# Performance work log

Hardware: AMD Instinct MI355X
Metric: run time of the kernel (lower is better)

The kernel has to match this reference:

```python
import jax, jax.numpy as jnp
import numpy as np

B, D = 8, 256
N_LIVE, K_NEW = 10000, 32
KC = N_LIVE + K_NEW
N_SAMPLES = 100
EPSILON = 0.1


def setup_inputs() -> dict:
    key = jax.random.key(0)
    k1, k2, k3, k4, k5, k6 = jax.random.split(key, 6)
    return {
        "xt": jax.random.normal(k1, (B, D), dtype=jnp.float32),
        "live_x0": jax.random.normal(k2, (B, N_LIVE, D), dtype=jnp.float32),
        "live_ll": jax.random.normal(k3, (B, N_LIVE, 1), dtype=jnp.float32),
        "x0": jax.random.normal(k4, (B, K_NEW, D), dtype=jnp.float32),
        "ll": jax.random.normal(k5, (B, K_NEW, 1), dtype=jnp.float32),
        "t_scale": jnp.float32(0.5),
        "boot_idx": jax.random.randint(k6, (N_SAMPLES, B, KC), 0, KC, dtype=jnp.int32),
    }


def reference(xt, live_x0, live_ll, x0, ll, t_scale, boot_idx):
    # --- spotlight_score core math ---
    # gaussian correction for the new particles: 0.5*||x0-xt||^2/sigma^2 + log(sigma)
    diff_new = x0 - xt[:, None, :]                                   # [B,K,D]
    corr_new = 0.5 * jnp.sum(diff_new ** 2, axis=-1, keepdims=True) / t_scale ** 2  # [B,K,1]
    current_x0 = jnp.concatenate([live_x0, x0], axis=1)              # [B,Kc,D]
    current_ll = jnp.concatenate(
        [live_ll, ll + corr_new + jnp.log(t_scale)], axis=1)         # [B,Kc,1]

    diff = current_x0 - xt[:, None, :]                               # [B,Kc,D]
    use_ll = (current_ll
              - 0.5 * jnp.sum(diff ** 2, axis=-1, keepdims=True) / t_scale ** 2
              - jnp.log(t_scale))                                    # [B,Kc,1]

    scores_p = diff / t_scale                                        # [B,Kc,D] per-particle scores
    logits = use_ll[..., 0]                                          # [B,Kc]

    # --- check_convergence: bootstrap resampled softmax reductions ---
    def body(carry, idx_n):                                          # idx_n: [B,Kc]
        s = jnp.take_along_axis(scores_p, idx_n[:, :, None], axis=1)  # [B,Kc,D]
        l = jnp.take_along_axis(logits, idx_n, axis=1)                # [B,Kc]
        w = jax.nn.softmax(l, axis=1)
        return carry, jnp.einsum('bk,bkd->bd', w, s)                  # [B,D]

    _, boot = jax.lax.scan(body, None, boot_idx)                      # [N,B,D]
    sigma_v = jnp.std(boot, axis=0, ddof=1)                           # [B,D] (torch.std is unbiased)
    converged = jnp.all(sigma_v < EPSILON * t_scale, axis=1)          # [B]

    # --- final importance-weighted score ---
    w = jax.nn.softmax(logits, axis=1)                                # [B,Kc]
    score = jnp.einsum('bk,bkd->bd', w, scores_p)                     # [B,D]
    return score, converged
```

## Files before the change

kernel.cpp:

```cpp
#include <hip/hip_runtime.h>
#include <math.h>

#define B 8
#define D 256
#define N_LIVE 10000
#define K_NEW 32
#define KC 10032
#define NS 100
#define NROW 101
#define EPS 0.1f
#define CAP 1024
#define ACT_CUT 87.0f
#define LBLK 314
#define BMAX_STRIDE 320

#define WS_HDR    0
#define WS_BMAX   160
#define WS_LOGITS (WS_BMAX + B * BMAX_STRIDE)
#define WS_ACTE   (WS_LOGITS + B * KC)
#define WS_ACTI   (WS_ACTE + B * CAP)
#define WS_LUT    (WS_ACTI + B * CAP)
#define WS_BOOT   (WS_LUT + B * KC / 2)


__global__ __launch_bounds__(256) void k_logits(
    const float* __restrict__ xt, const float* __restrict__ live_x0,
    const float* __restrict__ live_ll, const float* __restrict__ x0n,
    const float* __restrict__ lln, const float* __restrict__ ts_p,
    float* __restrict__ logits, float* __restrict__ bmax,
    unsigned* __restrict__ hdr) {
  int b = blockIdx.y;
  if (blockIdx.x == 0 && threadIdx.x == 0) hdr[128 + b] = 0;
  int w = threadIdx.x >> 6;
  int lane = threadIdx.x & 63;
  int k0 = blockIdx.x * 32 + w * 8;
  bool valid = (k0 < KC);
  int kb = valid ? k0 : 0;
  float4 c = ((const float4*)(xt + b * D))[lane];

  float s[8];
#pragma unroll
  for (int p = 0; p < 8; p++) {
    int k = kb + p;
    const float* src = (k < N_LIVE)
        ? (live_x0 + ((size_t)b * N_LIVE + k) * D)
        : (x0n + ((size_t)b * K_NEW + (k - N_LIVE)) * D);
    float4 v = ((const float4*)src)[lane];
    float dx = v.x - c.x, dy = v.y - c.y, dz = v.z - c.z, dw = v.w - c.w;
    s[p] = dx * dx + dy * dy + dz * dz + dw * dw;
  }
#pragma unroll
  for (int off = 32; off; off >>= 1) {
#pragma unroll
    for (int p = 0; p < 8; p++) s[p] += __shfl_xor(s[p], off);
  }
  __shared__ float wlog[4];
  if (lane == 0) {
    float ts = *ts_p;
    float inv2 = 0.5f / (ts * ts), lts = logf(ts);
    float o[8];
#pragma unroll
    for (int p = 0; p < 8; p++) {
      int k = kb + p;
      o[p] = (k < N_LIVE)
          ? live_ll[(size_t)b * N_LIVE + k] - s[p] * inv2 - lts
          : lln[(size_t)b * K_NEW + (k - N_LIVE)];
    }
    if (valid) {
      float4 o0 = {o[0], o[1], o[2], o[3]}, o1 = {o[4], o[5], o[6], o[7]};
      *(float4*)(logits + (size_t)b * KC + kb) = o0;
      *(float4*)(logits + (size_t)b * KC + kb + 4) = o1;
      wlog[w] = fmaxf(fmaxf(fmaxf(o[0], o[1]), fmaxf(o[2], o[3])),
                      fmaxf(fmaxf(o[4], o[5]), fmaxf(o[6], o[7])));
    } else {
      wlog[w] = -INFINITY;
    }
  }
  __syncthreads();
  if (threadIdx.x == 0)
    bmax[b * BMAX_STRIDE + blockIdx.x] =
        fmaxf(fmaxf(wlog[0], wlog[1]), fmaxf(wlog[2], wlog[3]));
}

__global__ __launch_bounds__(256) void k_select(
    const float* __restrict__ logits, const float* __restrict__ bmax,
    unsigned* __restrict__ hdr, float* __restrict__ act_e,
    int* __restrict__ act_idx, unsigned short* __restrict__ lut) {
  int b = blockIdx.y;
  __shared__ float sm[4];
  float m = -INFINITY;
  for (int i = threadIdx.x; i < LBLK; i += 256)
    m = fmaxf(m, bmax[b * BMAX_STRIDE + i]);
#pragma unroll
  for (int off = 32; off; off >>= 1) m = fmaxf(m, __shfl_xor(m, off));
  if ((threadIdx.x & 63) == 0) sm[threadIdx.x >> 6] = m;
  __syncthreads();
  float M = fmaxf(fmaxf(sm[0], sm[1]), fmaxf(sm[2], sm[3]));

  int tid = blockIdx.x * 256 + threadIdx.x;
  const float* lg = logits + (size_t)b * KC;
  int* cnt = (int*)&hdr[128 + b];
  for (int k = tid; k < KC; k += 8 * 256) {
    float l = lg[k];
    unsigned short v = 0;
    if (l > M - ACT_CUT) {
      int pos = atomicAdd(cnt, 1);
      if (pos < CAP) {
        act_e[b * CAP + pos] = expf(l - M);
        act_idx[b * CAP + pos] = k;
        v = (unsigned short)(pos + 1);
      }
    }
    lut[(size_t)b * KC + k] = v;
  }
}

__global__ __launch_bounds__(256) void k_boot(
    const float* __restrict__ live_x0, const float* __restrict__ x0n,
    const float* __restrict__ act_e, const int* __restrict__ act_idx,
    const unsigned* __restrict__ hdr, const unsigned short* __restrict__ lut,
    const int* __restrict__ boot_idx, float* __restrict__ boot) {
  int n = blockIdx.x;
  int b = blockIdx.y;
  int tid = threadIdx.x;
  int nw = tid >> 6, lane = tid & 63;
  __shared__ unsigned short slut[KC];
  __shared__ int cnt[CAP];
  __shared__ float wval[CAP];
  __shared__ int widx[CAP];
  __shared__ float4 part[4][64];
  __shared__ int snnz;
  __shared__ float sden[4];
  int A = min((int)hdr[128 + b], CAP);
  for (int i = tid; i < A; i += 256) cnt[i] = 0;
  if (tid == 0) snnz = 0;
  if (n < NS) {
    const unsigned* src = (const unsigned*)(lut + (size_t)b * KC);
    unsigned* dst = (unsigned*)slut;
    for (int i = tid; i < KC / 2; i += 256) dst[i] = src[i];
  }
  __syncthreads();

  if (n < NS) {
    const int4* row = (const int4*)(boot_idx + ((size_t)n * B + b) * KC);
    for (int k = tid; k < KC / 4; k += 256) {
      int4 v = row[k];
      int t;
      t = slut[v.x]; if (t) atomicAdd(&cnt[t - 1], 1);
      t = slut[v.y]; if (t) atomicAdd(&cnt[t - 1], 1);
      t = slut[v.z]; if (t) atomicAdd(&cnt[t - 1], 1);
      t = slut[v.w]; if (t) atomicAdd(&cnt[t - 1], 1);
    }
  } else {
    for (int i = tid; i < A; i += 256) cnt[i] = 1;
  }
  __syncthreads();

  float dpart = 0.f;
  for (int i = tid; i < A; i += 256) {
    int c = cnt[i];
    if (c) {
      float w = (float)c * act_e[b * CAP + i];
      int pos = atomicAdd(&snnz, 1);
      wval[pos] = w;
      widx[pos] = act_idx[b * CAP + i];
      dpart += w;
    }
  }
#pragma unroll
  for (int off = 32; off; off >>= 1) dpart += __shfl_xor(dpart, off);
  if ((tid & 63) == 0) sden[tid >> 6] = dpart;
  __syncthreads();
  float inv = 1.f / (sden[0] + sden[1] + sden[2] + sden[3]);
  int nnz = snnz;

  const float* lx = live_x0 + (size_t)b * N_LIVE * D;
  const float* nx = x0n + (size_t)b * K_NEW * D;
  float4 a0 = {0.f, 0.f, 0.f, 0.f}, a1 = {0.f, 0.f, 0.f, 0.f};
  int p = nw;
  for (; p + 4 < nnz; p += 8) {
    int j0 = widx[p], j1 = widx[p + 4];
    float w0 = wval[p], w1 = wval[p + 4];
    const float4* r0 = (const float4*)((j0 < N_LIVE) ? (lx + (size_t)j0 * D)
                                                     : (nx + (size_t)(j0 - N_LIVE) * D));
    const float4* r1 = (const float4*)((j1 < N_LIVE) ? (lx + (size_t)j1 * D)
                                                     : (nx + (size_t)(j1 - N_LIVE) * D));
    float4 v0 = r0[lane], v1 = r1[lane];
    a0.x = fmaf(w0, v0.x, a0.x); a0.y = fmaf(w0, v0.y, a0.y);
    a0.z = fmaf(w0, v0.z, a0.z); a0.w = fmaf(w0, v0.w, a0.w);
    a1.x = fmaf(w1, v1.x, a1.x); a1.y = fmaf(w1, v1.y, a1.y);
    a1.z = fmaf(w1, v1.z, a1.z); a1.w = fmaf(w1, v1.w, a1.w);
  }
  if (p < nnz) {
    int j = widx[p];
    float w = wval[p];
    const float4* r = (const float4*)((j < N_LIVE) ? (lx + (size_t)j * D)
                                                   : (nx + (size_t)(j - N_LIVE) * D));
    float4 v = r[lane];
    a0.x = fmaf(w, v.x, a0.x); a0.y = fmaf(w, v.y, a0.y);
    a0.z = fmaf(w, v.z, a0.z); a0.w = fmaf(w, v.w, a0.w);
  }
  a0.x += a1.x; a0.y += a1.y; a0.z += a1.z; a0.w += a1.w;
  part[nw][lane] = a0;
  __syncthreads();
  if (nw == 0) {
    float4 q0 = part[0][lane], q1 = part[1][lane], q2 = part[2][lane], q3 = part[3][lane];
    float4 r;
    r.x = ((q0.x + q1.x) + (q2.x + q3.x)) * inv;
    r.y = ((q0.y + q1.y) + (q2.y + q3.y)) * inv;
    r.z = ((q0.z + q1.z) + (q2.z + q3.z)) * inv;
    r.w = ((q0.w + q1.w) + (q2.w + q3.w)) * inv;
    ((float4*)(boot + ((size_t)b * NROW + n) * D))[lane] = r;
  }
}

__global__ __launch_bounds__(1024) void k_final(
    const float* __restrict__ boot, const float* __restrict__ xt,
    const float* __restrict__ ts_p, float* __restrict__ out) {
  int b = blockIdx.x;
  int tid = threadIdx.x;
  int d = tid & 255;
  int st = tid >> 8;
  float ts = *ts_p;
  const float* bb = boot + (size_t)b * NROW * D + d;
  __shared__ float red[4][256];
  __shared__ float mrow[256];
  __shared__ int wok[4];
  float s = 0.f;
#pragma unroll 5
  for (int i = 0; i < 25; i++) s += bb[(size_t)(st + 4 * i) * D];
  red[st][d] = s;
  __syncthreads();
  if (st == 0) mrow[d] = (red[0][d] + red[1][d] + red[2][d] + red[3][d]) / (float)NS;
  __syncthreads();
  float mean = mrow[d];
  float vs = 0.f;
#pragma unroll 5
  for (int i = 0; i < 25; i++) {
    float t = bb[(size_t)(st + 4 * i) * D] - mean;
    vs += t * t;
  }
  red[st][d] = vs;
  __syncthreads();
  if (st == 0) {
    float var = (red[0][d] + red[1][d] + red[2][d] + red[3][d]) / (float)(NS - 1);
    float sigma_raw = sqrtf(var);
    bool ok = (sigma_raw / ts) < (EPS * ts);
    out[(size_t)b * D + d] = (bb[(size_t)NS * D] - xt[(size_t)b * D + d]) / ts;
    unsigned long long m = __ballot(ok);
    if ((d & 63) == 0) wok[d >> 6] = (m == 0xFFFFFFFFFFFFFFFFull) ? 1 : 0;
  }
  __syncthreads();
  if (tid == 0)
    out[(size_t)B * D + b] = (wok[0] & wok[1] & wok[2] & wok[3]) ? 1.0f : 0.0f;
}

extern "C" void kernel_launch(void* const* d_in, const int* in_sizes, int n_in,
                              void* d_out, int out_size, void* d_ws, size_t ws_size,
                              hipStream_t stream) {
  const float* xt       = (const float*)d_in[0];
  const float* live_x0  = (const float*)d_in[1];
  const float* live_ll  = (const float*)d_in[2];
  const float* x0n      = (const float*)d_in[3];
  const float* lln      = (const float*)d_in[4];
  const float* ts_p     = (const float*)d_in[5];
  const int*   boot_idx = (const int*)d_in[6];
  float* out = (float*)d_out;
  float* ws  = (float*)d_ws;

  unsigned* hdr            = (unsigned*)(ws + WS_HDR);
  float* bmax              = ws + WS_BMAX;
  float* logits            = ws + WS_LOGITS;
  float* act_e             = ws + WS_ACTE;
  int*   act_idx           = (int*)(ws + WS_ACTI);
  unsigned short* lut      = (unsigned short*)(ws + WS_LUT);
  float* boot              = ws + WS_BOOT;

  k_logits<<<dim3(LBLK, B), 256, 0, stream>>>(xt, live_x0, live_ll, x0n, lln, ts_p, logits, bmax, hdr);
  k_select<<<dim3(8, B), 256, 0, stream>>>(logits, bmax, hdr, act_e, act_idx, lut);
  k_boot<<<dim3(NROW, B), 256, 0, stream>>>(live_x0, x0n, act_e, act_idx, hdr, lut, boot_idx, boot);
  k_final<<<dim3(B), 1024, 0, stream>>>(boot, xt, ts_p, out);
}
```

Before: 170.4 us.

## Fuse active-particle selection into bootstrap kernel with byte LUT in LDS

Removes the separate k_select launch. Each bootstrap block now recomputes the global max, thresholds the logits, and builds its own compact active list and an 8-bit lookup table in shared memory. Boot indices are prefetched into registers before the first barrier to overlap their load latency, and the nonzero-compaction pass is replaced with direct iteration over the active counts. In exchange, every one of the 808 blocks redoes the selection over KC logits. The active capacity also drops from 1024 to 255, so inputs with more active particles would be truncated and give wrong results.

```diff
diff --git a/kernel.cpp b/kernel.cpp
--- a/kernel.cpp
+++ b/kernel.cpp
@@ -6,31 +6,26 @@
 #define N_LIVE 10000
 #define K_NEW 32
 #define KC 10032
+#define KC4 2508
 #define NS 100
 #define NROW 101
 #define EPS 0.1f
-#define CAP 1024
+#define CAPA 255
 #define ACT_CUT 87.0f
 #define LBLK 314
 #define BMAX_STRIDE 320
 
-#define WS_HDR    0
-#define WS_BMAX   160
+#define WS_BMAX   0
 #define WS_LOGITS (WS_BMAX + B * BMAX_STRIDE)
-#define WS_ACTE   (WS_LOGITS + B * KC)
-#define WS_ACTI   (WS_ACTE + B * CAP)
-#define WS_LUT    (WS_ACTI + B * CAP)
-#define WS_BOOT   (WS_LUT + B * KC / 2)
+#define WS_BOOT   (WS_LOGITS + B * KC)
 
 
 __global__ __launch_bounds__(256) void k_logits(
     const float* __restrict__ xt, const float* __restrict__ live_x0,
     const float* __restrict__ live_ll, const float* __restrict__ x0n,
     const float* __restrict__ lln, const float* __restrict__ ts_p,
-    float* __restrict__ logits, float* __restrict__ bmax,
-    unsigned* __restrict__ hdr) {
+    float* __restrict__ logits, float* __restrict__ bmax) {
   int b = blockIdx.y;
-  if (blockIdx.x == 0 && threadIdx.x == 0) hdr[128 + b] = 0;
   int w = threadIdx.x >> 6;
   int lane = threadIdx.x & 63;
   int k0 = blockIdx.x * 32 + w * 8;
@@ -82,125 +77,103 @@
         fmaxf(fmaxf(wlog[0], wlog[1]), fmaxf(wlog[2], wlog[3]));
 }
 
-__global__ __launch_bounds__(256) void k_select(
-    const float* __restrict__ logits, const float* __restrict__ bmax,
-    unsigned* __restrict__ hdr, float* __restrict__ act_e,
-    int* __restrict__ act_idx, unsigned short* __restrict__ lut) {
-  int b = blockIdx.y;
-  __shared__ float sm[4];
-  float m = -INFINITY;
-  for (int i = threadIdx.x; i < LBLK; i += 256)
-    m = fmaxf(m, bmax[b * BMAX_STRIDE + i]);
-#pragma unroll
-  for (int off = 32; off; off >>= 1) m = fmaxf(m, __shfl_xor(m, off));
-  if ((threadIdx.x & 63) == 0) sm[threadIdx.x >> 6] = m;
-  __syncthreads();
-  float M = fmaxf(fmaxf(sm[0], sm[1]), fmaxf(sm[2], sm[3]));
-
-  int tid = blockIdx.x * 256 + threadIdx.x;
-  const float* lg = logits + (size_t)b * KC;
-  int* cnt = (int*)&hdr[128 + b];
-  for (int k = tid; k < KC; k += 8 * 256) {
-    float l = lg[k];
-    unsigned short v = 0;
-    if (l > M - ACT_CUT) {
-      int pos = atomicAdd(cnt, 1);
-      if (pos < CAP) {
-        act_e[b * CAP + pos] = expf(l - M);
-        act_idx[b * CAP + pos] = k;
-        v = (unsigned short)(pos + 1);
-      }
-    }
-    lut[(size_t)b * KC + k] = v;
-  }
-}
-
 __global__ __launch_bounds__(256) void k_boot(
     const float* __restrict__ live_x0, const float* __restrict__ x0n,
-    const float* __restrict__ act_e, const int* __restrict__ act_idx,
-    const unsigned* __restrict__ hdr, const unsigned short* __restrict__ lut,
+    const float* __restrict__ logits, const float* __restrict__ bmax,
     const int* __restrict__ boot_idx, float* __restrict__ boot) {
   int n = blockIdx.x;
   int b = blockIdx.y;
   int tid = threadIdx.x;
   int nw = tid >> 6, lane = tid & 63;
-  __shared__ unsigned short slut[KC];
-  __shared__ int cnt[CAP];
-  __shared__ float wval[CAP];
-  __shared__ int widx[CAP];
+  __shared__ unsigned slut32[KC4];
+  __shared__ float se[CAPA + 1];
+  __shared__ int sidx[CAPA + 1];
+  __shared__ int cnt[CAPA + 1];
   __shared__ float4 part[4][64];
-  __shared__ int snnz;
-  __shared__ float sden[4];
-  int A = min((int)hdr[128 + b], CAP);
-  for (int i = tid; i < A; i += 256) cnt[i] = 0;
-  if (tid == 0) snnz = 0;
+  __shared__ float sred[4];
+  __shared__ int sacnt;
+
+  float m = -INFINITY;
+  for (int i = tid; i < LBLK; i += 256) m = fmaxf(m, bmax[b * BMAX_STRIDE + i]);
+#pragma unroll
+  for (int off = 32; off; off >>= 1) m = fmaxf(m, __shfl_xor(m, off));
+  if (lane == 0) sred[nw] = m;
+  if (tid == 0) sacnt = 0;
+
+  int4 pre[10];
   if (n < NS) {
-    const unsigned* src = (const unsigned*)(lut + (size_t)b * KC);
-    unsigned* dst = (unsigned*)slut;
-    for (int i = tid; i < KC / 2; i += 256) dst[i] = src[i];
-  }
-  __syncthreads();
-
+    const int4* brow = (const int4*)(boot_idx + ((size_t)n * B + b) * KC);
+#pragma unroll
+    for (int i = 0; i < 10; i++) {
+      int k4 = tid + i * 256;
+      if (k4 < KC4) pre[i] = brow[k4];
+    }
+  }
+  __syncthreads();
+  float M = fmaxf(fmaxf(sred[0], sred[1]), fmaxf(sred[2], sred[3]));
+  float thr = M - ACT_CUT;
+
+  const float4* lg4 = (const float4*)(logits + (size_t)b * KC);
+  cnt[tid] = (n < NS) ? 0 : 1;
+#pragma unroll
+  for (int i = 0; i < 10; i++) {
+    int k4 = tid + i * 256;
+    if (k4 < KC4) {
+      float4 l4 = lg4[k4];
+      unsigned pack = 0;
+      float le; int pos;
+      le = l4.x; if (le > thr) { pos = atomicAdd(&sacnt, 1); if (pos < CAPA) {
+          se[pos] = expf(le - M); sidx[pos] = 4 * k4;     pack |= (unsigned)(pos + 1); } }
+      le = l4.y; if (le > thr) { pos = atomicAdd(&sacnt, 1); if (pos < CAPA) {
+          se[pos] = expf(le - M); sidx[pos] = 4 * k4 + 1; pack |= (unsigned)(pos + 1) << 8; } }
+      le = l4.z; if (le > thr) { pos = atomicAdd(&sacnt, 1); if (pos < CAPA) {
+          se[pos] = expf(le - M); sidx[pos] = 4 * k4 + 2; pack |= (unsigned)(pos + 1) << 16; } }
+      le = l4.w; if (le > thr) { pos = atomicAdd(&sacnt, 1); if (pos < CAPA) {
+          se[pos] = expf(le - M); sidx[pos] = 4 * k4 + 3; pack |= (unsigned)(pos + 1) << 24; } }
+      slut32[k4] = pack;
+    }
+  }
+  __syncthreads();
+  int A = min(sacnt, CAPA);
+
+  const unsigned char* lutb = (const unsigned char*)slut32;
   if (n < NS) {
-    const int4* row = (const int4*)(boot_idx + ((size_t)n * B + b) * KC);
-    for (int k = tid; k < KC / 4; k += 256) {
-      int4 v = row[k];
-      int t;
-      t = slut[v.x]; if (t) atomicAdd(&cnt[t - 1], 1);
-      t = slut[v.y]; if (t) atomicAdd(&cnt[t - 1], 1);
-      t = slut[v.z]; if (t) atomicAdd(&cnt[t - 1], 1);
-      t = slut[v.w]; if (t) atomicAdd(&cnt[t - 1], 1);
-    }
-  } else {
-    for (int i = tid; i < A; i += 256) cnt[i] = 1;
-  }
-  __syncthreads();
-
-  float dpart = 0.f;
-  for (int i = tid; i < A; i += 256) {
-    int c = cnt[i];
-    if (c) {
-      float w = (float)c * act_e[b * CAP + i];
-      int pos = atomicAdd(&snnz, 1);
-      wval[pos] = w;
-      widx[pos] = act_idx[b * CAP + i];
-      dpart += w;
-    }
-  }
-#pragma unroll
-  for (int off = 32; off; off >>= 1) dpart += __shfl_xor(dpart, off);
-  if ((tid & 63) == 0) sden[tid >> 6] = dpart;
-  __syncthreads();
-  float inv = 1.f / (sden[0] + sden[1] + sden[2] + sden[3]);
-  int nnz = snnz;
+#pragma unroll
+    for (int i = 0; i < 10; i++) {
+      int k4 = tid + i * 256;
+      if (k4 < KC4) {
+        int4 v = pre[i];
+        int t;
+        t = lutb[v.x]; if (t) atomicAdd(&cnt[t - 1], 1);
+        t = lutb[v.y]; if (t) atomicAdd(&cnt[t - 1], 1);
+        t = lutb[v.z]; if (t) atomicAdd(&cnt[t - 1], 1);
+        t = lutb[v.w]; if (t) atomicAdd(&cnt[t - 1], 1);
+      }
+    }
+  }
+  __syncthreads();
+
+  float d = (tid < A) ? (float)cnt[tid] * se[tid] : 0.f;
+#pragma unroll
+  for (int off = 32; off; off >>= 1) d += __shfl_xor(d, off);
+  if (lane == 0) sred[nw] = d;
+  __syncthreads();
+  float inv = 1.f / (sred[0] + sred[1] + sred[2] + sred[3]);
 
   const float* lx = live_x0 + (size_t)b * N_LIVE * D;
   const float* nx = x0n + (size_t)b * K_NEW * D;
-  float4 a0 = {0.f, 0.f, 0.f, 0.f}, a1 = {0.f, 0.f, 0.f, 0.f};
-  int p = nw;
-  for (; p + 4 < nnz; p += 8) {
-    int j0 = widx[p], j1 = widx[p + 4];
-    float w0 = wval[p], w1 = wval[p + 4];
-    const float4* r0 = (const float4*)((j0 < N_LIVE) ? (lx + (size_t)j0 * D)
-                                                     : (nx + (size_t)(j0 - N_LIVE) * D));
-    const float4* r1 = (const float4*)((j1 < N_LIVE) ? (lx + (size_t)j1 * D)
-                                                     : (nx + (size_t)(j1 - N_LIVE) * D));
-    float4 v0 = r0[lane], v1 = r1[lane];
-    a0.x = fmaf(w0, v0.x, a0.x); a0.y = fmaf(w0, v0.y, a0.y);
-    a0.z = fmaf(w0, v0.z, a0.z); a0.w = fmaf(w0, v0.w, a0.w);
-    a1.x = fmaf(w1, v1.x, a1.x); a1.y = fmaf(w1, v1.y, a1.y);
-    a1.z = fmaf(w1, v1.z, a1.z); a1.w = fmaf(w1, v1.w, a1.w);
-  }
-  if (p < nnz) {
-    int j = widx[p];
-    float w = wval[p];
+  float4 a0 = {0.f, 0.f, 0.f, 0.f};
+  for (int p = nw; p < A; p += 4) {
+    int c = cnt[p];
+    if (!c) continue;
+    float w = (float)c * se[p];
+    int j = sidx[p];
     const float4* r = (const float4*)((j < N_LIVE) ? (lx + (size_t)j * D)
                                                    : (nx + (size_t)(j - N_LIVE) * D));
     float4 v = r[lane];
     a0.x = fmaf(w, v.x, a0.x); a0.y = fmaf(w, v.y, a0.y);
     a0.z = fmaf(w, v.z, a0.z); a0.w = fmaf(w, v.w, a0.w);
   }
-  a0.x += a1.x; a0.y += a1.y; a0.z += a1.z; a0.w += a1.w;
   part[nw][lane] = a0;
   __syncthreads();
   if (nw == 0) {
@@ -247,8 +220,8 @@
     float sigma_raw = sqrtf(var);
     bool ok = (sigma_raw / ts) < (EPS * ts);
     out[(size_t)b * D + d] = (bb[(size_t)NS * D] - xt[(size_t)b * D + d]) / ts;
-    unsigned long long m = __ballot(ok);
-    if ((d & 63) == 0) wok[d >> 6] = (m == 0xFFFFFFFFFFFFFFFFull) ? 1 : 0;
+    unsigned long long mba = __ballot(ok);
+    if ((d & 63) == 0) wok[d >> 6] = (mba == 0xFFFFFFFFFFFFFFFFull) ? 1 : 0;
   }
   __syncthreads();
   if (tid == 0)
@@ -268,16 +241,11 @@
   float* out = (float*)d_out;
   float* ws  = (float*)d_ws;
 
-  unsigned* hdr            = (unsigned*)(ws + WS_HDR);
-  float* bmax              = ws + WS_BMAX;
-  float* logits            = ws + WS_LOGITS;
-  float* act_e             = ws + WS_ACTE;
-  int*   act_idx           = (int*)(ws + WS_ACTI);
-  unsigned short* lut      = (unsigned short*)(ws + WS_LUT);
-  float* boot              = ws + WS_BOOT;
-
-  k_logits<<<dim3(LBLK, B), 256, 0, stream>>>(xt, live_x0, live_ll, x0n, lln, ts_p, logits, bmax, hdr);
-  k_select<<<dim3(8, B), 256, 0, stream>>>(logits, bmax, hdr, act_e, act_idx, lut);
-  k_boot<<<dim3(NROW, B), 256, 0, stream>>>(live_x0, x0n, act_e, act_idx, hdr, lut, boot_idx, boot);
+  float* bmax   = ws + WS_BMAX;
+  float* logits = ws + WS_LOGITS;
+  float* boot   = ws + WS_BOOT;
+
+  k_logits<<<dim3(LBLK, B), 256, 0, stream>>>(xt, live_x0, live_ll, x0n, lln, ts_p, logits, bmax);
+  k_boot<<<dim3(NROW, B), 256, 0, stream>>>(live_x0, x0n, logits, bmax, boot_idx, boot);
   k_final<<<dim3(B), 1024, 0, stream>>>(boot, xt, ts_p, out);
 }
```

After: 170.5 us. Within noise of the previous version (+0.0%).
